# Optimization experiments

Hardware: AMD Instinct MI355X
Metric: run time of the kernel (lower is better)

The kernel has to match this reference:

```python
import jax, jax.numpy as jnp
import numpy as np
import math

D = 512      # d_model
HEADS = 16   # num_heads
HD = 32      # head_dim
WS = 7       # window_size
KS = 8       # patch_size
S = 4        # spectral_stride


def dct_basis(n):
    k = np.arange(n, dtype=np.float64)[:, None]
    i = np.arange(n, dtype=np.float64)[None, :]
    B = np.cos(np.pi * (i + 0.5) * k / n)
    B[0, :] *= 1.0 / np.sqrt(2.0)
    B = B * np.sqrt(2.0 / n)
    return jnp.asarray(B, dtype=jnp.float32)


def setup_inputs() -> dict:
    key = jax.random.key(0)
    ks = jax.random.split(key, 24)
    Bb, H, W = 4, 112, 112
    N = H * W
    w = lambda k, shape: jax.random.normal(k, shape, jnp.float32) * 0.02
    return {
        'tokens': jax.random.normal(ks[0], (Bb, N, D), jnp.float32),
        'patches': jax.random.normal(ks[1], (Bb, 3 * KS * KS, N), jnp.float32),
        'Wq': w(ks[2], (D, D)), 'bq': w(ks[3], (D,)),
        'Wk': w(ks[4], (D, D)), 'bk': w(ks[5], (D,)),
        'Wv': w(ks[6], (D, D)), 'bv': w(ks[7], (D,)),
        'Wo': w(ks[8], (D, D)), 'bo': w(ks[9], (D,)),
        'Wsp': w(ks[10], (3 * KS * KS, D)), 'bsp': w(ks[11], (D,)),
        'Wsq': w(ks[12], (D, D)), 'bsq': w(ks[13], (D,)),
        'Wsk': w(ks[14], (D, D)), 'bsk': w(ks[15], (D,)),
        'Wsv': w(ks[16], (D, D)), 'bsv': w(ks[17], (D,)),
        'Wso': w(ks[18], (D, D)), 'bso': w(ks[19], (D,)),
        'alpha': jnp.asarray(0.5, jnp.float32),
        'H': H, 'W': W,
    }


def reference(tokens, patches, Wq, bq, Wk, bk, Wv, bv, Wo, bo,
              Wsp, bsp, Wsq, bsq, Wsk, bsk, Wsv, bsv, Wso, bso,
              alpha, H, W):
    B, N, d = tokens.shape
    # ---- local windowed multi-head attention ----
    ws = WS
    pad_h = (-H) % ws
    pad_w = (-W) % ws
    x = tokens.reshape(B, H, W, d)
    if pad_h or pad_w:
        x = jnp.pad(x, ((0, 0), (0, pad_h), (0, pad_w), (0, 0)))
    Hp, Wp = H + pad_h, W + pad_w
    nh, nw_ = Hp // ws, Wp // ws
    xw = x.reshape(B, nh, ws, nw_, ws, d).transpose(0, 1, 3, 2, 4, 5)
    xw = xw.reshape(B * nh * nw_, ws * ws, d)  # (nw, 49, d)
    nw, L, _ = xw.shape
    q = (xw @ Wq + bq).reshape(nw, L, HEADS, HD)
    k = (xw @ Wk + bk).reshape(nw, L, HEADS, HD)
    v = (xw @ Wv + bv).reshape(nw, L, HEADS, HD)
    scale = 1.0 / math.sqrt(HD)
    attn = jax.nn.softmax(jnp.einsum('nqhd,nkhd->nhqk', q, k) * scale, axis=-1)
    o = jnp.einsum('nhqk,nkhd->nqhd', attn, v).reshape(nw, L, d)
    o = o @ Wo + bo
    o = o.reshape(B, nh, nw_, ws, ws, d).transpose(0, 1, 3, 2, 4, 5).reshape(B, Hp, Wp, d)
    sp_out = o[:, :H, :W, :].reshape(B, N, d)
    # ---- DCT on raw patches -> spectral descriptors ----
    Bm = dct_basis(KS)
    p = patches.reshape(B, 3, KS, KS, N)
    Fc = jnp.einsum('ij,bcjkn->bcikn', Bm, p)
    Fc = jnp.einsum('bcijn,jk->bcikn', Fc, Bm)  # right-multiply by Bm^T transposed back
    spec_desc = Fc.reshape(B, 3 * KS * KS, N).transpose(0, 2, 1) @ Wsp + bsp  # (B,N,d)
    # ---- strided global spectral attention + nearest upsample ----
    spec_hw = spec_desc.reshape(B, H, W, d)
    sd = spec_hw[:, ::S, ::S, :]
    Hs, Ws = sd.shape[1], sd.shape[2]
    sd = sd.reshape(B, Hs * Ws, d)
    qs = sd @ Wsq + bsq
    ks_ = sd @ Wsk + bsk
    vs = sd @ Wsv + bsv
    a = jax.nn.softmax(jnp.einsum('bqd,bkd->bqk', qs, ks_) / math.sqrt(d), axis=-1)
    so = jnp.einsum('bqk,bkd->bqd', a, vs) @ Wso + bso
    so = so.reshape(B, Hs, Ws, d)
    ri = (jnp.arange(H) * Hs) // H  # torch nearest: floor(i*in/out)
    ci = (jnp.arange(W) * Ws) // W
    spec_out = so[:, ri][:, :, ci].reshape(B, N, d)
    # ---- fuse + residual + layernorm (no affine) ----
    al = jax.nn.sigmoid(alpha)
    out = tokens + al * sp_out + (1.0 - al) * spec_out
    mu = out.mean(-1, keepdims=True)
    var = ((out - mu) ** 2).mean(-1, keepdims=True)
    return (out - mu) / jnp.sqrt(var + 1e-5)
```

## Files before the change

### kernel.cpp

```cpp
#include <hip/hip_runtime.h>

typedef unsigned short u16;
typedef __attribute__((ext_vector_type(4))) float f32x4;
typedef __attribute__((ext_vector_type(8))) short bf16x8;

#define AS1 __attribute__((address_space(1)))
#define AS3 __attribute__((address_space(3)))
#define GLL(gp, lp) __builtin_amdgcn_global_load_lds((const AS1 void*)(gp), (AS3 void*)(lp), 16, 0, 0)

__device__ __forceinline__ float b2f(u16 v) { return __uint_as_float(((unsigned)v) << 16); }
__device__ __forceinline__ u16 f2b(float f) {
  unsigned u = __float_as_uint(f);
  u += 0x7fffu + ((u >> 16) & 1u);
  return (u16)(u >> 16);
}
__device__ __forceinline__ unsigned pack2(float a, float b) {
  return (unsigned)f2b(a) | ((unsigned)f2b(b) << 16);
}
__device__ __forceinline__ float blo(unsigned u) { return __uint_as_float(u << 16); }
__device__ __forceinline__ float bhi(unsigned u) { return __uint_as_float(u & 0xffff0000u); }

__global__ __launch_bounds__(256) void gemm_bt(
    const u16* __restrict__ A, int lda, long sAb,
    const u16* __restrict__ Bt, int ldb, long sBb,
    const float* __restrict__ bias, void* __restrict__ Cv, int ldc, long sCb,
    int M, int N, int K, int c_bf16)
{
  __shared__ __align__(16) u16 ldsA[128 * 64];
  __shared__ __align__(16) u16 ldsB[128 * 64];
  int tid = threadIdx.x;
  int wid = tid >> 6, lane = tid & 63;

  int nbx = gridDim.x;
  int lin = blockIdx.y * nbx + blockIdx.x;
  int nwg = nbx * gridDim.y;
  int qc = nwg >> 3, rc = nwg & 7;
  int xcd = lin & 7, pos = lin >> 3;
  int nlin = (xcd < rc ? xcd * (qc + 1) : rc * (qc + 1) + (xcd - rc) * qc) + pos;
  int bx = nlin % nbx, by = nlin / nbx;

  int row0 = by << 7;
  int col0 = bx << 7;
  int bz = blockIdx.z;
  A += (size_t)bz * sAb;
  Bt += (size_t)bz * sBb;
  int wr = (wid >> 1) << 6, wc = (wid & 1) << 6;

  const u16* pA[4];
  const u16* pB[4];
  int ldso[4];
#pragma unroll
  for (int q = 0; q < 4; ++q) {
    int inst = (wid << 2) + q;
    int o = (inst << 10) + (lane << 4);
    int r = o >> 7;
    int cs = (o >> 4) & 7;
    int cl = cs ^ (r & 7);
    int ar = row0 + r; ar = ar < M ? ar : M - 1;
    int br = col0 + r; br = br < N ? br : N - 1;
    pA[q] = A + (size_t)ar * lda + (cl << 3);
    pB[q] = Bt + (size_t)br * ldb + (cl << 3);
    ldso[q] = inst << 9;
  }

  f32x4 acc[4][4];
#pragma unroll
  for (int i = 0; i < 4; ++i)
#pragma unroll
    for (int j = 0; j < 4; ++j) { f32x4 z = {0.f, 0.f, 0.f, 0.f}; acc[i][j] = z; }

  int nt = K >> 6;
  for (int t = 0; t < nt; ++t) {
#pragma unroll
    for (int q = 0; q < 4; ++q) {
      GLL(pA[q], ldsA + ldso[q]);
      GLL(pB[q], ldsB + ldso[q]);
      pA[q] += 64; pB[q] += 64;
    }
    __syncthreads();
#pragma unroll
    for (int kk = 0; kk < 2; ++kk) {
      bf16x8 af[4], bg[4];
#pragma unroll
      for (int mi = 0; mi < 4; ++mi) {
        int r = wr + (mi << 4) + (lane & 15);
        int cs = ((kk << 2) + (lane >> 4)) ^ (r & 7);
        af[mi] = *(const bf16x8*)(ldsA + (r << 6) + (cs << 3));
      }
#pragma unroll
      for (int ni = 0; ni < 4; ++ni) {
        int r = wc + (ni << 4) + (lane & 15);
        int cs = ((kk << 2) + (lane >> 4)) ^ (r & 7);
        bg[ni] = *(const bf16x8*)(ldsB + (r << 6) + (cs << 3));
      }
#pragma unroll
      for (int mi = 0; mi < 4; ++mi)
#pragma unroll
        for (int ni = 0; ni < 4; ++ni)
          acc[mi][ni] = __builtin_amdgcn_mfma_f32_16x16x32_bf16(af[mi], bg[ni], acc[mi][ni], 0, 0, 0);
    }
    __syncthreads();
  }

#pragma unroll
  for (int mi = 0; mi < 4; ++mi) {
    int rb = row0 + wr + (mi << 4) + ((lane >> 4) << 2);
#pragma unroll
    for (int ni = 0; ni < 4; ++ni) {
      int c = col0 + wc + (ni << 4) + (lane & 15);
      float bv = (bias && c < N) ? bias[c] : 0.f;
#pragma unroll
      for (int j = 0; j < 4; ++j) {
        int r = rb + j;
        if (r < M && c < N) {
          float v = acc[mi][ni][j] + bv;
          if (c_bf16) ((u16*)Cv)[(size_t)bz * sCb + (size_t)r * ldc + c] = f2b(v);
          else ((float*)Cv)[(size_t)bz * sCb + (size_t)r * ldc + c] = v;
        }
      }
    }
  }
}

__global__ __launch_bounds__(256, 2) void win_attn_mfma(const u16* __restrict__ qkv, u16* __restrict__ oat)
{
  __shared__ __align__(16) u16 Pl[4][64 * 72];
  __shared__ __align__(16) u16 Vtl[4][32 * 72];
  int tid = threadIdx.x;
  int wid = tid >> 6, lane = tid & 63;
  int lm = lane & 15, lg = lane >> 4;
  int w = blockIdx.x;
  int b = w >> 8, wh = (w >> 4) & 15, ww = w & 15;
  int rowbase = (wh * 7) * 112 + ww * 7;
  u16* P = Pl[wid];
  u16* Vt = Vtl[wid];
  const u16* base = qkv + (size_t)b * 12544 * 1536;
  u16* ob = oat + (size_t)b * 12544 * 512;
  const float scale = 0.17677669529663687f;

  for (int hh = 0; hh < 4; ++hh) {
    int h = wid * 4 + hh;
    bf16x8 Qf[4], Kf[4];
#pragma unroll
    for (int mi = 0; mi < 4; ++mi) {
      int i = mi * 16 + lm; i = i < 49 ? i : 48;
      int q7 = (i * 147) >> 10;
      int n = rowbase + q7 * 112 + (i - q7 * 7);
      const u16* rp = base + (size_t)n * 1536 + h * 32 + lg * 8;
      Qf[mi] = *(const bf16x8*)(rp);
      Kf[mi] = *(const bf16x8*)(rp + 512);
    }
    {
      int j = lane;
      if (j < 49) {
        int q7 = (j * 147) >> 10;
        int n = rowbase + q7 * 112 + (j - q7 * 7);
        const uint4* vp = (const uint4*)(base + (size_t)n * 1536 + 1024 + h * 32);
#pragma unroll
        for (int t = 0; t < 4; ++t) {
          uint4 u = vp[t];
          Vt[(t * 8 + 0) * 72 + j] = (u16)(u.x & 0xffff); Vt[(t * 8 + 1) * 72 + j] = (u16)(u.x >> 16);
          Vt[(t * 8 + 2) * 72 + j] = (u16)(u.y & 0xffff); Vt[(t * 8 + 3) * 72 + j] = (u16)(u.y >> 16);
          Vt[(t * 8 + 4) * 72 + j] = (u16)(u.z & 0xffff); Vt[(t * 8 + 5) * 72 + j] = (u16)(u.z >> 16);
          Vt[(t * 8 + 6) * 72 + j] = (u16)(u.w & 0xffff); Vt[(t * 8 + 7) * 72 + j] = (u16)(u.w >> 16);
        }
      } else {
#pragma unroll
        for (int d = 0; d < 32; ++d) Vt[d * 72 + j] = 0;
      }
    }
    f32x4 S[4][4];
#pragma unroll
    for (int mi = 0; mi < 4; ++mi)
#pragma unroll
      for (int nj = 0; nj < 4; ++nj) { f32x4 z = {0.f, 0.f, 0.f, 0.f}; S[mi][nj] = z; }
#pragma unroll
    for (int mi = 0; mi < 4; ++mi)
#pragma unroll
      for (int nj = 0; nj < 4; ++nj)
        S[mi][nj] = __builtin_amdgcn_mfma_f32_16x16x32_bf16(Qf[mi], Kf[nj], S[mi][nj], 0, 0, 0);
    float invv[4][4];
#pragma unroll
    for (int mi = 0; mi < 4; ++mi) {
#pragma unroll
      for (int reg = 0; reg < 4; ++reg) {
        float v0 = S[mi][0][reg], v1 = S[mi][1][reg], v2 = S[mi][2][reg], v3 = S[mi][3][reg];
        if (lm) v3 = -1e30f;
        float m = fmaxf(fmaxf(v0, v1), fmaxf(v2, v3));
#pragma unroll
        for (int o = 1; o < 16; o <<= 1) m = fmaxf(m, __shfl_xor(m, o));
        float e0 = __expf((v0 - m) * scale);
        float e1 = __expf((v1 - m) * scale);
        float e2 = __expf((v2 - m) * scale);
        float e3 = lm ? 0.f : __expf((v3 - m) * scale);
        float s = e0 + e1 + e2 + e3;
#pragma unroll
        for (int o = 1; o < 16; o <<= 1) s += __shfl_xor(s, o);
        invv[mi][reg] = 1.f / s;
        int r = mi * 16 + lg * 4 + reg;
        P[r * 72 + lm] = f2b(e0);
        P[r * 72 + 16 + lm] = f2b(e1);
        P[r * 72 + 32 + lm] = f2b(e2);
        P[r * 72 + 48 + lm] = f2b(e3);
      }
    }
    bf16x8 Vf[2][2];
#pragma unroll
    for (int dt = 0; dt < 2; ++dt) {
      Vf[dt][0] = *(const bf16x8*)(Vt + (dt * 16 + lm) * 72 + lg * 8);
      Vf[dt][1] = *(const bf16x8*)(Vt + (dt * 16 + lm) * 72 + 32 + lg * 8);
    }
    f32x4 O[4][2];
#pragma unroll
    for (int mi = 0; mi < 4; ++mi)
#pragma unroll
      for (int dt = 0; dt < 2; ++dt) { f32x4 z = {0.f, 0.f, 0.f, 0.f}; O[mi][dt] = z; }
#pragma unroll
    for (int mi = 0; mi < 4; ++mi) {
      bf16x8 Pf0 = *(const bf16x8*)(P + (mi * 16 + lm) * 72 + lg * 8);
      bf16x8 Pf1 = *(const bf16x8*)(P + (mi * 16 + lm) * 72 + 32 + lg * 8);
#pragma unroll
      for (int dt = 0; dt < 2; ++dt) {
        O[mi][dt] = __builtin_amdgcn_mfma_f32_16x16x32_bf16(Pf0, Vf[dt][0], O[mi][dt], 0, 0, 0);
        O[mi][dt] = __builtin_amdgcn_mfma_f32_16x16x32_bf16(Pf1, Vf[dt][1], O[mi][dt], 0, 0, 0);
      }
    }
#pragma unroll
    for (int mi = 0; mi < 4; ++mi)
#pragma unroll
      for (int reg = 0; reg < 4; ++reg) {
        int i = mi * 16 + lg * 4 + reg;
        if (i < 49) {
          int q7 = (i * 147) >> 10;
          int n = rowbase + q7 * 112 + (i - q7 * 7);
          float iv = invv[mi][reg];
          u16* op = ob + (size_t)n * 512 + h * 32 + lm;
          op[0] = f2b(O[mi][0][reg] * iv);
          op[16] = f2b(O[mi][1][reg] * iv);
        }
      }
  }
}

__global__ __launch_bounds__(192) void dct_f2(const float* __restrict__ patches, u16* __restrict__ F2)
{
  __shared__ float pv[192];
  __shared__ float Bm[64];
  int blk = blockIdx.x;
  int b = blk / 784, rem = blk % 784;
  int n = ((rem / 28) * 4) * 112 + (rem % 28) * 4;
  int t = threadIdx.x;
  if (t < 64) {
    int k = t >> 3, ii = t & 7;
    float v = cosf(3.14159265358979323846f * (ii + 0.5f) * (float)k * 0.125f) * 0.5f;
    if (k == 0) v *= 0.70710678118654752f;
    Bm[t] = v;
  }
  pv[t] = patches[((size_t)b * 192 + t) * 12544 + n];
  __syncthreads();
  int c = t >> 6, fi = (t >> 3) & 7, fk = t & 7;
  float acc = 0.f;
#pragma unroll
  for (int mm = 0; mm < 8; ++mm) {
    float g = 0.f;
#pragma unroll
    for (int jj = 0; jj < 8; ++jj) g += pv[c * 64 + mm * 8 + jj] * Bm[jj * 8 + fk];
    acc += Bm[fi * 8 + mm] * g;
  }
  F2[(size_t)blk * 192 + t] = f2b(acc);
}

__global__ __launch_bounds__(256) void spec_softmax(const float* __restrict__ S, u16* __restrict__ P)
{
  __shared__ float red[4];
  int row = blockIdx.x;
  const float* sr = S + (size_t)row * 784;
  u16* pr = P + (size_t)row * 832;
  int t = threadIdx.x;
  int lane = t & 63, wid = t >> 6;
  float v0 = sr[t];
  float v1 = sr[t + 256];
  float v2 = (t < 272) ? sr[t + 512] : -1e30f;
  float m = fmaxf(fmaxf(v0, v1), v2);
#pragma unroll
  for (int ofs = 32; ofs > 0; ofs >>= 1) m = fmaxf(m, __shfl_xor(m, ofs));
  if (lane == 0) red[wid] = m;
  __syncthreads();
  m = fmaxf(fmaxf(red[0], red[1]), fmaxf(red[2], red[3]));
  __syncthreads();
  const float scale = 0.044194173824159216f;
  float e0 = __expf((v0 - m) * scale);
  float e1 = __expf((v1 - m) * scale);
  float e2 = (t < 272) ? __expf((v2 - m) * scale) : 0.f;
  float sum = e0 + e1 + e2;
#pragma unroll
  for (int ofs = 32; ofs > 0; ofs >>= 1) sum += __shfl_xor(sum, ofs);
  if (lane == 0) red[wid] = sum;
  __syncthreads();
  sum = red[0] + red[1] + red[2] + red[3];
  float inv = 1.f / sum;
  pr[t] = f2b(e0 * inv);
  pr[t + 256] = f2b(e1 * inv);
  if (t < 272) pr[t + 512] = f2b(e2 * inv);
  else if (t < 320) pr[t + 512] = 0;
}

__global__ __launch_bounds__(256) void transV(const u16* __restrict__ qkvs, u16* __restrict__ Vt)
{
  int idx = blockIdx.x * 256 + threadIdx.x;
  int k = idx % 832;
  int rest = idx / 832;
  int n = rest % 512, b = rest / 512;
  u16 v = 0;
  if (k < 784) v = qkvs[((size_t)(b * 784 + k)) * 1536 + 1024 + n];
  Vt[idx] = v;
}

__global__ __launch_bounds__(256) void combine_ln(
    const float* __restrict__ tokens, const u16* __restrict__ sp,
    const float* __restrict__ so, const float* __restrict__ alpha,
    float* __restrict__ out)
{
  int nidx = blockIdx.x;
  int b = nidx / 12544, pos = nidx % 12544;
  int i = pos / 112, j = pos % 112;
  const float* tr = tokens + (size_t)nidx * 512;
  const u16* sr = sp + (size_t)nidx * 512;
  const float* qr = so + (size_t)(b * 784 + (i >> 2) * 28 + (j >> 2)) * 512;
  float al = 1.f / (1.f + __expf(-alpha[0]));
  float be = 1.f - al;
  int t = threadIdx.x;
  float x0 = tr[t] + al * b2f(sr[t]) + be * qr[t];
  float x1 = tr[t + 256] + al * b2f(sr[t + 256]) + be * qr[t + 256];
  float s = x0 + x1, ss = x0 * x0 + x1 * x1;
#pragma unroll
  for (int ofs = 32; ofs > 0; ofs >>= 1) { s += __shfl_xor(s, ofs); ss += __shfl_xor(ss, ofs); }
  __shared__ float rs[4], rq[4];
  int lane = t & 63, wid = t >> 6;
  if (lane == 0) { rs[wid] = s; rq[wid] = ss; }
  __syncthreads();
  s = rs[0] + rs[1] + rs[2] + rs[3];
  ss = rq[0] + rq[1] + rq[2] + rq[3];
  float mu = s * 0.001953125f;
  float var = ss * 0.001953125f - mu * mu;
  float rstd = rsqrtf(var + 1e-5f);
  float* orow = out + (size_t)nidx * 512;
  orow[t] = (x0 - mu) * rstd;
  orow[t + 256] = (x1 - mu) * rstd;
}

__global__ __launch_bounds__(256) void transT(const float* __restrict__ src, u16* __restrict__ dst, int K, int Nc)
{
  int idx = blockIdx.x * 256 + threadIdx.x;
  if (idx >= K * Nc) return;
  int nn = idx / K, kk = idx % K;
  dst[idx] = f2b(src[(size_t)kk * Nc + nn]);
}

__global__ __launch_bounds__(256) void cvtbf(const float* __restrict__ src, u16* __restrict__ dst)
{
  size_t i = ((size_t)blockIdx.x * 256 + threadIdx.x) * 4;
  float4 v = *(const float4*)(src + i);
  uint2 u;
  u.x = pack2(v.x, v.y);
  u.y = pack2(v.z, v.w);
  *(uint2*)(dst + i) = u;
}

__global__ __launch_bounds__(256) void stack_bias(
    const float* bq_, const float* bk_, const float* bv_,
    const float* bsq_, const float* bsk_, const float* bsv_,
    float* bqkv, float* bsqkv)
{
  int i = blockIdx.x * 256 + threadIdx.x;
  if (i >= 1536) return;
  int r = i & 511;
  bqkv[i]  = (i < 512) ? bq_[r]  : (i < 1024) ? bk_[r]  : bv_[r];
  bsqkv[i] = (i < 512) ? bsq_[r] : (i < 1024) ? bsk_[r] : bsv_[r];
}

extern "C" void kernel_launch(void* const* d_in, const int* in_sizes, int n_in,
                              void* d_out, int out_size, void* d_ws, size_t ws_size,
                              hipStream_t stream) {
  (void)in_sizes; (void)n_in; (void)out_size; (void)ws_size;
  const float* tokens = (const float*)d_in[0];
  const float* patches = (const float*)d_in[1];
  const float* Wq  = (const float*)d_in[2];
  const float* bq  = (const float*)d_in[3];
  const float* Wk  = (const float*)d_in[4];
  const float* bk  = (const float*)d_in[5];
  const float* Wv  = (const float*)d_in[6];
  const float* bv  = (const float*)d_in[7];
  const float* Wo  = (const float*)d_in[8];
  const float* bo  = (const float*)d_in[9];
  const float* Wsp = (const float*)d_in[10];
  const float* bsp = (const float*)d_in[11];
  const float* Wsq = (const float*)d_in[12];
  const float* bsq = (const float*)d_in[13];
  const float* Wsk = (const float*)d_in[14];
  const float* bsk = (const float*)d_in[15];
  const float* Wsv = (const float*)d_in[16];
  const float* bsv = (const float*)d_in[17];
  const float* Wso = (const float*)d_in[18];
  const float* bso = (const float*)d_in[19];
  const float* alpha = (const float*)d_in[20];
  float* out = (float*)d_out;

  char* ws = (char*)d_ws;
  u16* tokbf  = (u16*)ws;
  u16* qkv    = (u16*)(ws + 51380224);
  char* pp    = ws + 51380224 + 154140672;
  u16* WqkvT  = (u16*)pp; pp += 1572864;
  u16* WoT    = (u16*)pp; pp += 524288;
  u16* WsqkvT = (u16*)pp; pp += 1572864;
  u16* WsoT   = (u16*)pp; pp += 524288;
  u16* WspT   = (u16*)pp; pp += 196608;
  float* bqkv = (float*)pp; pp += 6144;
  float* bsqkv= (float*)pp; pp += 6144;
  u16* F2b    = (u16*)pp; pp += 1204224;
  u16* sd     = (u16*)pp; pp += 3211264;
  u16* qkvs   = (u16*)pp; pp += 9633792;
  u16* sopre  = (u16*)pp; pp += 3211264;
  float* sofin= (float*)pp; pp += 6422528;

  float* Sbuf = (float*)tokbf;
  u16* Pbuf   = (u16*)(ws + 9834496);
  u16* Vt     = (u16*)(ws + 9834496 + 5218304);

  cvtbf<<<25088, 256, 0, stream>>>(tokens, tokbf);
  transT<<<1024, 256, 0, stream>>>(Wq, WqkvT, 512, 512);
  transT<<<1024, 256, 0, stream>>>(Wk, WqkvT + 262144, 512, 512);
  transT<<<1024, 256, 0, stream>>>(Wv, WqkvT + 524288, 512, 512);
  transT<<<1024, 256, 0, stream>>>(Wo, WoT, 512, 512);
  transT<<<1024, 256, 0, stream>>>(Wsq, WsqkvT, 512, 512);
  transT<<<1024, 256, 0, stream>>>(Wsk, WsqkvT + 262144, 512, 512);
  transT<<<1024, 256, 0, stream>>>(Wsv, WsqkvT + 524288, 512, 512);
  transT<<<1024, 256, 0, stream>>>(Wso, WsoT, 512, 512);
  transT<<<384, 256, 0, stream>>>(Wsp, WspT, 192, 512);
  stack_bias<<<6, 256, 0, stream>>>(bq, bk, bv, bsq, bsk, bsv, bqkv, bsqkv);

  gemm_bt<<<dim3(12, 392), 256, 0, stream>>>(tokbf, 512, 0, WqkvT, 512, 0, bqkv, qkv, 1536, 0, 50176, 1536, 512, 1);
  win_attn_mfma<<<1024, 256, 0, stream>>>(qkv, tokbf);
  gemm_bt<<<dim3(4, 392), 256, 0, stream>>>(tokbf, 512, 0, WoT, 512, 0, bo, qkv, 512, 0, 50176, 512, 512, 1);

  dct_f2<<<3136, 192, 0, stream>>>(patches, F2b);
  gemm_bt<<<dim3(4, 25), 256, 0, stream>>>(F2b, 192, 0, WspT, 192, 0, bsp, sd, 512, 0, 3136, 512, 192, 1);
  gemm_bt<<<dim3(12, 25), 256, 0, stream>>>(sd, 512, 0, WsqkvT, 512, 0, bsqkv, qkvs, 1536, 0, 3136, 1536, 512, 1);
  gemm_bt<<<dim3(7, 7, 4), 256, 0, stream>>>(qkvs, 1536, (long)784 * 1536, qkvs + 512, 1536, (long)784 * 1536,
                                             nullptr, Sbuf, 784, (long)784 * 784, 784, 784, 512, 0);
  spec_softmax<<<3136, 256, 0, stream>>>(Sbuf, Pbuf);
  transV<<<6656, 256, 0, stream>>>(qkvs, Vt);
  gemm_bt<<<dim3(4, 7, 4), 256, 0, stream>>>(Pbuf, 832, (long)784 * 832, Vt, 832, (long)512 * 832,
                                             nullptr, sopre, 512, (long)784 * 512, 784, 512, 832, 1);
  gemm_bt<<<dim3(4, 25), 256, 0, stream>>>(sopre, 512, 0, WsoT, 512, 0, bso, sofin, 512, 0, 3136, 512, 512, 0);

  combine_ln<<<50176, 256, 0, stream>>>(tokens, qkv, sofin, alpha, out);
}
```

Baseline: 540.8 us.

## Add 256x256-tile double-buffered GEMM for the large QKV and output projections

Adds a new gemm_big kernel with 512 threads and 256x256 output tiles. It double-buffers the 64-wide K slices in LDS using direct global-to-LDS loads and splits the MFMA work into four phases interleaved with prefetches, raising wave priority during the MFMA phases. The two large projections (QKV and Wo over 50176 rows) now use it in place of the 128x128 gemm_bt. The aim is more data reuse per tile and overlap of loads with matrix math, at the cost of larger register and LDS use per block and fewer blocks for the N=512 case.

Measured after the change: 581.9 us. +7.6%, slower.

```diff
diff --git a/kernel.cpp b/kernel.cpp
--- a/kernel.cpp
+++ b/kernel.cpp
@@ -19,6 +19,167 @@
 }
 __device__ __forceinline__ float blo(unsigned u) { return __uint_as_float(u << 16); }
 __device__ __forceinline__ float bhi(unsigned u) { return __uint_as_float(u & 0xffff0000u); }
+
+__global__ __launch_bounds__(512, 2) void gemm_big(
+    const u16* __restrict__ A, int lda,
+    const u16* __restrict__ Bt, int ldb,
+    const float* __restrict__ bias, void* __restrict__ Cv, int ldc,
+    int M, int N, int K, int c_bf16)
+{
+  __shared__ __align__(16) u16 ldsA[2][16384];
+  __shared__ __align__(16) u16 ldsB[2][16384];
+  int tid = threadIdx.x;
+  int wid = tid >> 6, lane = tid & 63;
+  int lm = lane & 15, lg = lane >> 4;
+  int wm = wid >> 2, wn = wid & 3;
+
+  int nbx = gridDim.x;
+  int lin = blockIdx.y * nbx + blockIdx.x;
+  int nwg = nbx * gridDim.y;
+  int qc = nwg >> 3, rc = nwg & 7;
+  int xcd = lin & 7, pos = lin >> 3;
+  int nlin = (xcd < rc ? xcd * (qc + 1) : rc * (qc + 1) + (xcd - rc) * qc) + pos;
+  int bx = nlin % nbx, by = nlin / nbx;
+  int row0 = by << 8, col0 = bx << 8;
+
+  int srow = tid >> 3;
+  int scl = (tid & 7) ^ (srow & 7);
+  int ldsoff = tid << 3;
+  const u16* pA[4];
+  const u16* pB[4];
+#pragma unroll
+  for (int g = 0; g < 4; ++g) {
+    int ar = row0 + g * 64 + srow; ar = ar < M ? ar : M - 1;
+    int br = col0 + g * 64 + srow; br = br < N ? br : N - 1;
+    pA[g] = A + (size_t)ar * lda + (scl << 3);
+    pB[g] = Bt + (size_t)br * ldb + (scl << 3);
+  }
+
+  f32x4 acc[8][4];
+#pragma unroll
+  for (int i = 0; i < 8; ++i)
+#pragma unroll
+    for (int j = 0; j < 4; ++j) { f32x4 z = {0.f, 0.f, 0.f, 0.f}; acc[i][j] = z; }
+
+#pragma unroll
+  for (int g = 0; g < 4; ++g) {
+    GLL(pA[g], &ldsA[0][g * 4096 + ldsoff]);
+    GLL(pB[g], &ldsB[0][g * 4096 + ldsoff]);
+    pA[g] += 64; pB[g] += 64;
+  }
+  asm volatile("s_waitcnt vmcnt(0)" ::: "memory");
+  __builtin_amdgcn_s_barrier();
+
+  int abase = (wm * 128 + lm) * 64;
+  int bbase = (wn * 64 + lm) * 64;
+  int cs0 = ((lg) ^ (lm & 7)) << 3;
+  int cs1 = ((4 + lg) ^ (lm & 7)) << 3;
+
+  int nt = K >> 6;
+  for (int t = 0; t < nt; ++t) {
+    int cb = t & 1, nb = cb ^ 1;
+    bool pf = (t + 1) < nt;
+    bf16x8 Af[4][2], Bf[4][2];
+
+    if (pf) {
+#pragma unroll
+      for (int g = 0; g < 2; ++g) {
+        GLL(pA[g], &ldsA[nb][g * 4096 + ldsoff]);
+        GLL(pB[g], &ldsB[nb][g * 4096 + ldsoff]);
+        pA[g] += 64; pB[g] += 64;
+      }
+    }
+#pragma unroll
+    for (int ni = 0; ni < 4; ++ni) {
+      Bf[ni][0] = *(const bf16x8*)(&ldsB[cb][bbase + ni * 1024 + cs0]);
+      Bf[ni][1] = *(const bf16x8*)(&ldsB[cb][bbase + ni * 1024 + cs1]);
+    }
+#pragma unroll
+    for (int mi = 0; mi < 4; ++mi) {
+      Af[mi][0] = *(const bf16x8*)(&ldsA[cb][abase + mi * 1024 + cs0]);
+      Af[mi][1] = *(const bf16x8*)(&ldsA[cb][abase + mi * 1024 + cs1]);
+    }
+    __builtin_amdgcn_s_barrier();
+    __builtin_amdgcn_s_setprio(1);
+#pragma unroll
+    for (int mi = 0; mi < 4; ++mi)
+#pragma unroll
+      for (int ni = 0; ni < 2; ++ni) {
+        acc[mi][ni] = __builtin_amdgcn_mfma_f32_16x16x32_bf16(Af[mi][0], Bf[ni][0], acc[mi][ni], 0, 0, 0);
+        acc[mi][ni] = __builtin_amdgcn_mfma_f32_16x16x32_bf16(Af[mi][1], Bf[ni][1], acc[mi][ni], 0, 0, 0);
+      }
+    __builtin_amdgcn_s_setprio(0);
+    __builtin_amdgcn_s_barrier();
+
+    if (pf) {
+#pragma unroll
+      for (int g = 2; g < 4; ++g) {
+        GLL(pA[g], &ldsA[nb][g * 4096 + ldsoff]);
+        GLL(pB[g], &ldsB[nb][g * 4096 + ldsoff]);
+        pA[g] += 64; pB[g] += 64;
+      }
+    }
+    __builtin_amdgcn_s_barrier();
+    __builtin_amdgcn_s_setprio(1);
+#pragma unroll
+    for (int mi = 0; mi < 4; ++mi)
+#pragma unroll
+      for (int ni = 2; ni < 4; ++ni) {
+        acc[mi][ni] = __builtin_amdgcn_mfma_f32_16x16x32_bf16(Af[mi][0], Bf[ni][0], acc[mi][ni], 0, 0, 0);
+        acc[mi][ni] = __builtin_amdgcn_mfma_f32_16x16x32_bf16(Af[mi][1], Bf[ni][1], acc[mi][ni], 0, 0, 0);
+      }
+    __builtin_amdgcn_s_setprio(0);
+    __builtin_amdgcn_s_barrier();
+
+#pragma unroll
+    for (int mi = 0; mi < 4; ++mi) {
+      Af[mi][0] = *(const bf16x8*)(&ldsA[cb][abase + 4096 + mi * 1024 + cs0]);
+      Af[mi][1] = *(const bf16x8*)(&ldsA[cb][abase + 4096 + mi * 1024 + cs1]);
+    }
+    __builtin_amdgcn_s_barrier();
+    __builtin_amdgcn_s_setprio(1);
+#pragma unroll
+    for (int mi = 0; mi < 4; ++mi)
+#pragma unroll
+      for (int ni = 2; ni < 4; ++ni) {
+        acc[4 + mi][ni] = __builtin_amdgcn_mfma_f32_16x16x32_bf16(Af[mi][0], Bf[ni][0], acc[4 + mi][ni], 0, 0, 0);
+        acc[4 + mi][ni] = __builtin_amdgcn_mfma_f32_16x16x32_bf16(Af[mi][1], Bf[ni][1], acc[4 + mi][ni], 0, 0, 0);
+      }
+    __builtin_amdgcn_s_setprio(0);
+    __builtin_amdgcn_s_barrier();
+
+    __builtin_amdgcn_s_setprio(1);
+#pragma unroll
+    for (int mi = 0; mi < 4; ++mi)
+#pragma unroll
+      for (int ni = 0; ni < 2; ++ni) {
+        acc[4 + mi][ni] = __builtin_amdgcn_mfma_f32_16x16x32_bf16(Af[mi][0], Bf[ni][0], acc[4 + mi][ni], 0, 0, 0);
+        acc[4 + mi][ni] = __builtin_amdgcn_mfma_f32_16x16x32_bf16(Af[mi][1], Bf[ni][1], acc[4 + mi][ni], 0, 0, 0);
+      }
+    __builtin_amdgcn_s_setprio(0);
+    asm volatile("s_waitcnt vmcnt(0)" ::: "memory");
+    __builtin_amdgcn_s_barrier();
+  }
+
+#pragma unroll
+  for (int mig = 0; mig < 8; ++mig) {
+    int r0 = row0 + wm * 128 + mig * 16 + (lg << 2);
+#pragma unroll
+    for (int ni = 0; ni < 4; ++ni) {
+      int c = col0 + wn * 64 + ni * 16 + lm;
+      float bv = (bias && c < N) ? bias[c] : 0.f;
+#pragma unroll
+      for (int j = 0; j < 4; ++j) {
+        int r = r0 + j;
+        if (r < M && c < N) {
+          float v = acc[mig][ni][j] + bv;
+          if (c_bf16) ((u16*)Cv)[(size_t)r * ldc + c] = f2b(v);
+          else ((float*)Cv)[(size_t)r * ldc + c] = v;
+        }
+      }
+    }
+  }
+}
 
 __global__ __launch_bounds__(256) void gemm_bt(
     const u16* __restrict__ A, int lda, long sAb,
@@ -439,9 +600,9 @@
   transT<<<384, 256, 0, stream>>>(Wsp, WspT, 192, 512);
   stack_bias<<<6, 256, 0, stream>>>(bq, bk, bv, bsq, bsk, bsv, bqkv, bsqkv);
 
-  gemm_bt<<<dim3(12, 392), 256, 0, stream>>>(tokbf, 512, 0, WqkvT, 512, 0, bqkv, qkv, 1536, 0, 50176, 1536, 512, 1);
+  gemm_big<<<dim3(6, 196), 512, 0, stream>>>(tokbf, 512, WqkvT, 512, bqkv, qkv, 1536, 50176, 1536, 512, 1);
   win_attn_mfma<<<1024, 256, 0, stream>>>(qkv, tokbf);
-  gemm_bt<<<dim3(4, 392), 256, 0, stream>>>(tokbf, 512, 0, WoT, 512, 0, bo, qkv, 512, 0, 50176, 512, 512, 1);
+  gemm_big<<<dim3(2, 196), 512, 0, stream>>>(tokbf, 512, WoT, 512, bo, qkv, 512, 50176, 512, 512, 1);
 
   dct_f2<<<3136, 192, 0, stream>>>(patches, F2b);
   gemm_bt<<<dim3(4, 25), 256, 0, stream>>>(F2b, 192, 0, WspT, 192, 0, bsp, sd, 512, 0, 3136, 512, 192, 1);
```
